# Optimization experiments

Hardware: AMD Instinct MI355X
Metric: run time of the kernel (lower is better)

Reference implementation:

```python
import jax, jax.numpy as jnp
import numpy as np

NEG = -10000.0
SLOPE = 0.2


def setup_inputs() -> dict:
    key = jax.random.key(0)
    k1, k2, k3, k4, k5 = jax.random.split(key, 5)
    B, N, F_in, F_out = 8, 2048, 512, 512
    text = jax.random.normal(k1, (B, N, F_in), dtype=jnp.float32)
    adj = jax.random.randint(k2, (B, N, N), 0, 2, dtype=jnp.int32)
    sc = 1.0 / np.sqrt(F_in)
    W = jax.random.normal(k3, (F_in, F_out), dtype=jnp.float32) * sc
    b = jnp.zeros((F_out,), dtype=jnp.float32)
    a_src = jax.random.normal(k4, (F_out,), dtype=jnp.float32) * sc
    a_dst = jax.random.normal(k5, (F_out,), dtype=jnp.float32) * sc
    return {"text": text, "adj": adj, "W": W, "b": b, "a_src": a_src, "a_dst": a_dst}


def reference(text, adj, W, b, a_src, a_dst):
    # hidden: [B, N, F_out]
    hidden = jnp.einsum("bnf,fo->bno", text, W) + b
    s = jnp.einsum("bno,o->bn", hidden, a_src)  # src score per node
    d = jnp.einsum("bno,o->bn", hidden, a_dst)  # dst score per node
    scores = s[:, :, None] + d[:, None, :]      # [B, N, N]
    scores = jnp.where(scores >= 0, scores, SLOPE * scores)  # LeakyReLU
    # faithful to original: masked_fill where adj.bool() is True
    scores = jnp.where(adj.astype(bool), NEG, scores)
    attn = jax.nn.softmax(scores, axis=-1)
    return jnp.einsum("bnm,bmo->bno", attn, hidden)
```

## Files before the change

kernel.cpp:

```cpp
#include <hip/hip_runtime.h>
#include <stdint.h>

#define NB 8
#define NN 2048
#define NF 512
#define TOTN (NB * NN)

typedef unsigned short u16;
typedef short bf16x8 __attribute__((ext_vector_type(8)));
typedef float f32x4 __attribute__((ext_vector_type(4)));

__device__ __forceinline__ u16 f2bf(float x) {
  unsigned u = __float_as_uint(x);
  unsigned r = 0x7FFFu + ((u >> 16) & 1u);
  return (u16)((u + r) >> 16);
}

__device__ __forceinline__ void gl2lds16(const void* g, void* l) {
  __builtin_amdgcn_global_load_lds((const __attribute__((address_space(1))) void*)g,
                                   (__attribute__((address_space(3))) void*)l,
                                   16, 0, 0);
}


__global__ __launch_bounds__(256) void conv_kernel(
    const float* __restrict__ text, const float* __restrict__ W,
    u16* __restrict__ text_bf, u16* __restrict__ Wt) {
  int blk = blockIdx.x;
  if (blk < 8192) {
    int idx = blk * 256 + threadIdx.x;
    float4 v = ((const float4*)text)[idx];
    ushort4 o;
    o.x = f2bf(v.x); o.y = f2bf(v.y); o.z = f2bf(v.z); o.w = f2bf(v.w);
    ((ushort4*)text_bf)[idx] = o;
  } else {
    int t = (blk - 8192) * 256 + threadIdx.x;
    int o = t >> 9, f = t & 511;
    Wt[o * NF + f] = f2bf(W[f * NF + o]);
  }
}

__global__ __launch_bounds__(256) void pack_kernel(
    const int* __restrict__ adj, uint32_t* __restrict__ bm) {
  int gid = blockIdx.x * 256 + threadIdx.x;
  const int4* p = (const int4*)(adj + (size_t)gid * 32);
  uint32_t bits = 0;
#pragma unroll
  for (int c = 0; c < 8; ++c) {
    int4 a = p[c];
    bits |= (uint32_t)(a.x != 0) << (c * 4 + 0);
    bits |= (uint32_t)(a.y != 0) << (c * 4 + 1);
    bits |= (uint32_t)(a.z != 0) << (c * 4 + 2);
    bits |= (uint32_t)(a.w != 0) << (c * 4 + 3);
  }
  bm[gid] = bits;
}

__global__ __launch_bounds__(256) void gemm1_kernel(
    const u16* __restrict__ A,
    const u16* __restrict__ Bt,
    const float* __restrict__ bias, const float* __restrict__ a_src,
    const float* __restrict__ a_dst, u16* __restrict__ hS,
    float* __restrict__ s, float* __restrict__ d) {
  __shared__ u16 Alds[128 * 32];
  __shared__ u16 Blds[128 * 32];

  const int bn = blockIdx.x, bm_ = blockIdx.y;
  const int t = threadIdx.x, wave = t >> 6, lane = t & 63;
  const int wm = (wave >> 1) * 64, wn = (wave & 1) * 64;

  f32x4 acc[4][4];
#pragma unroll
  for (int i = 0; i < 4; ++i)
#pragma unroll
    for (int j = 0; j < 4; ++j) acc[i][j] = (f32x4){0.f, 0.f, 0.f, 0.f};

  const int rowA0 = bm_ * 128, rowB0 = bn * 128;
  const int srow = (lane >> 2);
  const int scol = (lane & 3) * 8;

  for (int kt = 0; kt < NF; kt += 32) {
#pragma unroll
    for (int q = 0; q < 2; ++q) {
      int r = wave * 32 + q * 16;
      gl2lds16(A + (size_t)(rowA0 + r + srow) * NF + (kt + scol), &Alds[r * 32]);
    }
#pragma unroll
    for (int q = 0; q < 2; ++q) {
      int r = wave * 32 + q * 16;
      gl2lds16(Bt + (size_t)(rowB0 + r + srow) * NF + (kt + scol), &Blds[r * 32]);
    }
    __syncthreads();

    const int fr = lane & 15;
    const int k0 = (lane >> 4) * 8;
    bf16x8 af[4], bfr[4];
#pragma unroll
    for (int i = 0; i < 4; ++i)
      af[i] = *(const bf16x8*)&Alds[(wm + i * 16 + fr) * 32 + k0];
#pragma unroll
    for (int j = 0; j < 4; ++j)
      bfr[j] = *(const bf16x8*)&Blds[(wn + j * 16 + fr) * 32 + k0];
#pragma unroll
    for (int i = 0; i < 4; ++i)
#pragma unroll
      for (int j = 0; j < 4; ++j)
        acc[i][j] = __builtin_amdgcn_mfma_f32_16x16x32_bf16(af[i], bfr[j],
                                                            acc[i][j], 0, 0, 0);
    __syncthreads();
  }

  const int quad = lane >> 4, ln16 = lane & 15;
  float sa[4] = {0.f, 0.f, 0.f, 0.f}, da[4] = {0.f, 0.f, 0.f, 0.f};
#pragma unroll
  for (int i = 0; i < 4; ++i) {
    int m0 = bm_ * 128 + wm + i * 16 + quad * 4;
#pragma unroll
    for (int r = 0; r < 4; ++r) {
      int m = m0 + r;
      float bv = bias[m];
      float asv = a_src[m], adv = a_dst[m];
      int oh = m >> 8, och = (m >> 4) & 15, rc = m & 15;
#pragma unroll
      for (int j = 0; j < 4; ++j) {
        int n = bn * 128 + wn + j * 16 + ln16;
        float h = acc[i][j][r] + bv;
        int zz = n >> 11, nz = n & 2047;
        int kc = nz >> 5, kin = nz & 31;
        size_t off = ((((size_t)zz * 2 + oh) * 64 + kc) << 13)
                     + (och << 9)
                     + ((size_t)(rc * 4 + ((kin >> 3) ^ ((rc >> 1) & 3))) << 3)
                     + (kin & 7);
        hS[off] = f2bf(h);
        sa[j] = fmaf(h, asv, sa[j]);
        da[j] = fmaf(h, adv, da[j]);
      }
    }
  }
#pragma unroll
  for (int j = 0; j < 4; ++j) {
    float v = sa[j] + __shfl_xor(sa[j], 16, 64);
    v += __shfl_xor(v, 32, 64);
    float w2 = da[j] + __shfl_xor(da[j], 16, 64);
    w2 += __shfl_xor(w2, 32, 64);
    if (quad == 0) {
      int n = bn * 128 + wn + j * 16 + ln16;
      atomicAdd(&s[n], v);
      atomicAdd(&d[n], w2);
    }
  }
}

__global__ __launch_bounds__(256, 2) void fused_attn_kernel(
    const uint32_t* __restrict__ bm, const float* __restrict__ s,
    const float* __restrict__ d, const u16* __restrict__ hS,
    float* __restrict__ out) {
  __shared__ u16 Blds[16384];
  __shared__ u16 Plds[4096];
  __shared__ float lpart[256];
  __shared__ float linv_lds[64];

  const int z = blockIdx.z, oh = blockIdx.y;
  const int i0 = blockIdx.x * 64;
  const int t = threadIdx.x, wave = t >> 6, lane = t & 63;
  const int quad = lane >> 4, ln16 = lane & 15;

  const int pr = t >> 2;
  const int ko = (t & 3) * 16;
  const float si = s[z * NN + i0 + pr];
  const uint32_t* bmrow = bm + (size_t)(z * NN + i0 + pr) * 64;
  const float* db = d + z * NN;

  const char* slabB = (const char*)hS + (size_t)(z * 2 + oh) * 1048576;

  f32x4 acc[4][4];
#pragma unroll
  for (int i = 0; i < 4; ++i)
#pragma unroll
    for (int j = 0; j < 4; ++j) acc[i][j] = (f32x4){0.f, 0.f, 0.f, 0.f};

  uint32_t bw = bmrow[ko >> 5];
  float4 dv[4];
#pragma unroll
  for (int c = 0; c < 4; ++c) dv[c] = *(const float4*)&db[ko + c * 4];

  const int fslot = ln16 * 4 + (quad ^ ((ln16 >> 1) & 3));
  const int prc = pr & 15, pch = pr >> 4;
  const int ph = ko >> 5, pq0 = (ko >> 3) & 3;
  char* pbase = (char*)Plds + ph * 4096 + pch * 1024;
  char* pdst0 = pbase + (prc * 4 + (pq0 ^ ((prc >> 1) & 3))) * 16;
  char* pdst1 = pbase + (prc * 4 + ((pq0 + 1) ^ ((prc >> 1) & 3))) * 16;

  float lsum = 0.f;

  for (int kt = 0; kt < NN; kt += 64) {
    uint32_t bits16 = (bw >> (ko & 16)) & 0xFFFFu;
    u16 pk[16];
#pragma unroll
    for (int cc = 0; cc < 4; ++cc) {
      float4 dq = dv[cc];
#pragma unroll
      for (int e = 0; e < 4; ++e) {
        float dj = (e == 0) ? dq.x : (e == 1) ? dq.y : (e == 2) ? dq.z : dq.w;
        float x = si + dj;
        float xm = fmaxf(x, 0.2f * x);
        float p = ((bits16 >> (cc * 4 + e)) & 1u) ? 0.f : __expf(xm);
        lsum += p;
        pk[cc * 4 + e] = f2bf(p);
      }
    }

    __syncthreads();

    *(int4*)pdst0 = *(int4*)&pk[0];
    *(int4*)pdst1 = *(int4*)&pk[8];

    {
      const char* gB = slabB + (size_t)kt * 512;
#pragma unroll
      for (int c = 0; c < 8; ++c) {
        int boff = (c * 4 + wave) * 1024;
        gl2lds16(gB + boff + lane * 16, (char*)Blds + boff);
      }
    }
    __syncthreads();

    if (kt + 64 < NN) {
      bw = bmrow[((kt + 64) >> 5) + (ko >> 5)];
#pragma unroll
      for (int c = 0; c < 4; ++c)
        dv[c] = *(const float4*)&db[kt + 64 + ko + c * 4];
    }

#pragma unroll
    for (int h = 0; h < 2; ++h) {
      bf16x8 af[4], bfv[4];
#pragma unroll
      for (int i = 0; i < 4; ++i)
        af[i] = *(const bf16x8*)((const char*)Plds + h * 4096 + i * 1024 + fslot * 16);
#pragma unroll
      for (int j = 0; j < 4; ++j)
        bfv[j] = *(const bf16x8*)((const char*)Blds + h * 16384 +
                                  (wave * 4 + j) * 1024 + fslot * 16);
#pragma unroll
      for (int i = 0; i < 4; ++i)
#pragma unroll
        for (int j = 0; j < 4; ++j)
          acc[i][j] = __builtin_amdgcn_mfma_f32_16x16x32_bf16(af[i], bfv[j],
                                                              acc[i][j], 0, 0, 0);
    }
  }

  lpart[pr * 4 + (t & 3)] = lsum;
  __syncthreads();
  if (t < 64) {
    const float* lp = &lpart[t * 4];
    linv_lds[t] = 1.0f / ((lp[0] + lp[1]) + (lp[2] + lp[3]));
  }
  __syncthreads();

#pragma unroll
  for (int i = 0; i < 4; ++i) {
#pragma unroll
    for (int r = 0; r < 4; ++r) {
      int m = i * 16 + quad * 4 + r;
      float sc = linv_lds[m];
      float* ob = out + ((size_t)(z * NN) + i0 + m) * NF + oh * 256 + wave * 64;
#pragma unroll
      for (int j = 0; j < 4; ++j) ob[j * 16 + ln16] = acc[i][j][r] * sc;
    }
  }
}

extern "C" void kernel_launch(void* const* d_in, const int* in_sizes, int n_in,
                              void* d_out, int out_size, void* d_ws,
                              size_t ws_size, hipStream_t stream) {
  const float* text  = (const float*)d_in[0];
  const int*   adj   = (const int*)d_in[1];
  const float* W     = (const float*)d_in[2];
  const float* bias  = (const float*)d_in[3];
  const float* a_src = (const float*)d_in[4];
  const float* a_dst = (const float*)d_in[5];
  float* out = (float*)d_out;

  char* ws = (char*)d_ws;
  u16*      text_bf = (u16*)(ws + 0);
  u16*      Wt      = (u16*)(ws + 16777216);
  u16*      hS      = (u16*)(ws + 17301504);
  float*    s       = (float*)(ws + 34078720);
  float*    d       = (float*)(ws + 34144256);
  uint32_t* bmask   = (uint32_t*)(ws + 34209792);

  hipMemsetAsync(s, 0, 131072, stream);

  conv_kernel<<<9216, 256, 0, stream>>>(text, W, text_bf, Wt);
  pack_kernel<<<4096, 256, 0, stream>>>(adj, bmask);

  gemm1_kernel<<<dim3(128, 4, 1), 256, 0, stream>>>(Wt, text_bf, bias, a_src,
                                                    a_dst, hS, s, d);

  fused_attn_kernel<<<dim3(NN / 64, 2, NB), 256, 0, stream>>>(bmask, s, d, hS,
                                                              out);
}
```

Measured before the change: 299.7 us.

## Double-buffer hidden tiles in attention loop and merge prep kernels with memset

The attention kernel now keeps two LDS buffers for the hidden-state tile. It prefetches the next tile with global_load_lds while the current one feeds MFMA, and uses explicit vmcnt waits and raw barriers in place of __syncthreads. The conversion, adjacency-packing and s/d zeroing work are merged into one prep kernel, which drops a memset and a launch. LDS use doubles, which may reduce occupancy at two blocks per CU. The hand-tuned waitcnt value depends on how the compiler orders instructions.

```diff
diff --git a/kernel.cpp b/kernel.cpp
--- a/kernel.cpp
+++ b/kernel.cpp
@@ -23,9 +23,11 @@
 }
 
 
-__global__ __launch_bounds__(256) void conv_kernel(
+__global__ __launch_bounds__(256) void prep_kernel(
     const float* __restrict__ text, const float* __restrict__ W,
-    u16* __restrict__ text_bf, u16* __restrict__ Wt) {
+    const int* __restrict__ adj, u16* __restrict__ text_bf,
+    u16* __restrict__ Wt, uint32_t* __restrict__ bm,
+    float* __restrict__ sd) {
   int blk = blockIdx.x;
   if (blk < 8192) {
     int idx = blk * 256 + threadIdx.x;
@@ -33,27 +35,29 @@
     ushort4 o;
     o.x = f2bf(v.x); o.y = f2bf(v.y); o.z = f2bf(v.z); o.w = f2bf(v.w);
     ((ushort4*)text_bf)[idx] = o;
-  } else {
+  } else if (blk < 9216) {
     int t = (blk - 8192) * 256 + threadIdx.x;
     int o = t >> 9, f = t & 511;
     Wt[o * NF + f] = f2bf(W[f * NF + o]);
-  }
-}
-
-__global__ __launch_bounds__(256) void pack_kernel(
-    const int* __restrict__ adj, uint32_t* __restrict__ bm) {
-  int gid = blockIdx.x * 256 + threadIdx.x;
-  const int4* p = (const int4*)(adj + (size_t)gid * 32);
-  uint32_t bits = 0;
-#pragma unroll
-  for (int c = 0; c < 8; ++c) {
-    int4 a = p[c];
-    bits |= (uint32_t)(a.x != 0) << (c * 4 + 0);
-    bits |= (uint32_t)(a.y != 0) << (c * 4 + 1);
-    bits |= (uint32_t)(a.z != 0) << (c * 4 + 2);
-    bits |= (uint32_t)(a.w != 0) << (c * 4 + 3);
-  }
-  bm[gid] = bits;
+  } else if (blk < 13312) {
+    int gid = (blk - 9216) * 256 + threadIdx.x;
+    const int4* p = (const int4*)(adj + (size_t)gid * 32);
+    uint32_t bits = 0;
+#pragma unroll
+    for (int c = 0; c < 8; ++c) {
+      int4 a = p[c];
+      bits |= (uint32_t)(a.x != 0) << (c * 4 + 0);
+      bits |= (uint32_t)(a.y != 0) << (c * 4 + 1);
+      bits |= (uint32_t)(a.z != 0) << (c * 4 + 2);
+      bits |= (uint32_t)(a.w != 0) << (c * 4 + 3);
+    }
+    bm[gid] = bits;
+  } else {
+    float4* p = (float4*)sd;
+#pragma unroll
+    for (int c = 0; c < 32; ++c)
+      p[c * 256 + threadIdx.x] = (float4){0.f, 0.f, 0.f, 0.f};
+  }
 }
 
 __global__ __launch_bounds__(256) void gemm1_kernel(
@@ -155,7 +159,7 @@
     const uint32_t* __restrict__ bm, const float* __restrict__ s,
     const float* __restrict__ d, const u16* __restrict__ hS,
     float* __restrict__ out) {
-  __shared__ u16 Blds[16384];
+  __shared__ u16 Blds[2][16384];
   __shared__ u16 Plds[4096];
   __shared__ float lpart[256];
   __shared__ float linv_lds[64];
@@ -178,11 +182,6 @@
   for (int i = 0; i < 4; ++i)
 #pragma unroll
     for (int j = 0; j < 4; ++j) acc[i][j] = (f32x4){0.f, 0.f, 0.f, 0.f};
-
-  uint32_t bw = bmrow[ko >> 5];
-  float4 dv[4];
-#pragma unroll
-  for (int c = 0; c < 4; ++c) dv[c] = *(const float4*)&db[ko + c * 4];
 
   const int fslot = ln16 * 4 + (quad ^ ((ln16 >> 1) & 3));
   const int prc = pr & 15, pch = pr >> 4;
@@ -191,7 +190,19 @@
   char* pdst0 = pbase + (prc * 4 + (pq0 ^ ((prc >> 1) & 3))) * 16;
   char* pdst1 = pbase + (prc * 4 + ((pq0 + 1) ^ ((prc >> 1) & 3))) * 16;
 
+  uint32_t bw = bmrow[ko >> 5];
+  float4 dv[4];
+#pragma unroll
+  for (int c = 0; c < 4; ++c) dv[c] = *(const float4*)&db[ko + c * 4];
+  __builtin_amdgcn_sched_barrier(0);
+#pragma unroll
+  for (int c = 0; c < 8; ++c) {
+    int boff = (c * 4 + wave) * 1024;
+    gl2lds16(slabB + boff + lane * 16, (char*)&Blds[0][0] + boff);
+  }
+
   float lsum = 0.f;
+  int buf = 0;
 
   for (int kt = 0; kt < NN; kt += 64) {
     uint32_t bits16 = (bw >> (ko & 16)) & 0xFFFFu;
@@ -210,28 +221,33 @@
       }
     }
 
-    __syncthreads();
+    bool more = (kt + 64 < NN);
+    if (more) {
+      bw = bmrow[((kt + 64) >> 5) + (ko >> 5)];
+#pragma unroll
+      for (int c = 0; c < 4; ++c)
+        dv[c] = *(const float4*)&db[kt + 64 + ko + c * 4];
+      __builtin_amdgcn_sched_barrier(0);
+      const char* gB = slabB + (size_t)(kt + 64) * 512;
+      char* bdst = (char*)&Blds[buf ^ 1][0];
+#pragma unroll
+      for (int c = 0; c < 8; ++c) {
+        int boff = (c * 4 + wave) * 1024;
+        gl2lds16(gB + boff + lane * 16, bdst + boff);
+      }
+    }
 
     *(int4*)pdst0 = *(int4*)&pk[0];
     *(int4*)pdst1 = *(int4*)&pk[8];
 
-    {
-      const char* gB = slabB + (size_t)kt * 512;
-#pragma unroll
-      for (int c = 0; c < 8; ++c) {
-        int boff = (c * 4 + wave) * 1024;
-        gl2lds16(gB + boff + lane * 16, (char*)Blds + boff);
-      }
-    }
-    __syncthreads();
-
-    if (kt + 64 < NN) {
-      bw = bmrow[((kt + 64) >> 5) + (ko >> 5)];
-#pragma unroll
-      for (int c = 0; c < 4; ++c)
-        dv[c] = *(const float4*)&db[kt + 64 + ko + c * 4];
-    }
-
+    if (more)
+      asm volatile("s_waitcnt vmcnt(13) lgkmcnt(0)" ::: "memory");
+    else
+      asm volatile("s_waitcnt vmcnt(0) lgkmcnt(0)" ::: "memory");
+    __builtin_amdgcn_s_barrier();
+    asm volatile("" ::: "memory");
+
+    const char* bbase = (const char*)&Blds[buf][0];
 #pragma unroll
     for (int h = 0; h < 2; ++h) {
       bf16x8 af[4], bfv[4];
@@ -240,7 +256,7 @@
         af[i] = *(const bf16x8*)((const char*)Plds + h * 4096 + i * 1024 + fslot * 16);
 #pragma unroll
       for (int j = 0; j < 4; ++j)
-        bfv[j] = *(const bf16x8*)((const char*)Blds + h * 16384 +
+        bfv[j] = *(const bf16x8*)(bbase + h * 16384 +
                                   (wave * 4 + j) * 1024 + fslot * 16);
 #pragma unroll
       for (int i = 0; i < 4; ++i)
@@ -249,6 +265,11 @@
           acc[i][j] = __builtin_amdgcn_mfma_f32_16x16x32_bf16(af[i], bfv[j],
                                                               acc[i][j], 0, 0, 0);
     }
+
+    asm volatile("" ::: "memory");
+    __builtin_amdgcn_s_barrier();
+    asm volatile("" ::: "memory");
+    buf ^= 1;
   }
 
   lpart[pr * 4 + (t & 3)] = lsum;
@@ -291,10 +312,7 @@
   float*    d       = (float*)(ws + 34144256);
   uint32_t* bmask   = (uint32_t*)(ws + 34209792);
 
-  hipMemsetAsync(s, 0, 131072, stream);
-
-  conv_kernel<<<9216, 256, 0, stream>>>(text, W, text_bf, Wt);
-  pack_kernel<<<4096, 256, 0, stream>>>(adj, bmask);
+  prep_kernel<<<13313, 256, 0, stream>>>(text, W, adj, text_bf, Wt, bmask, s);
 
   gemm1_kernel<<<dim3(128, 4, 1), 256, 0, stream>>>(Wt, text_bf, bias, a_src,
                                                     a_dst, hS, s, d);
```

New measurement: 299.0 us. About the same (-0.2%).
